# Performance work log

Measured on AMD Instinct MI355X. Metric: run time of the kernel, lower is better.

## Reference

```python
import jax, jax.numpy as jnp
import numpy as np

B, IN, OUT, L, R = 8192, 4096, 4096, 4, 128


def setup_inputs() -> dict:
    key = jax.random.key(0)
    ks = jax.random.split(key, 6)
    scale = 1.0 / np.sqrt(IN)
    return {
        "h_in": jax.random.normal(ks[0], (B, IN), dtype=jnp.float32),
        "S1s": jax.random.normal(ks[1], (L, IN, R), dtype=jnp.float32) * scale,
        "S2s": jax.random.normal(ks[2], (L, R, OUT), dtype=jnp.float32) * scale,
        "U1s": jax.random.normal(ks[3], (L, R, OUT), dtype=jnp.float32) / np.sqrt(R),
        "U2s": jax.random.normal(ks[4], (L, IN, R), dtype=jnp.float32) / np.sqrt(R),
        "bias": jax.random.normal(ks[5], (OUT,), dtype=jnp.float32) * scale,
    }


def reference(h_in, S1s, S2s, U1s, U2s, bias):
    l = S1s.shape[0]
    # term 1: x @ S1_i @ U1_i ; sketch to rank r then expand to out
    t1 = jnp.einsum("bi,lir->lbr", h_in, S1s)          # (l, B, r)
    y1 = jnp.einsum("lbr,lro->bo", t1, U1s)             # (B, out)
    # term 2: x @ U2_i @ S2_i
    t2 = jnp.einsum("bi,lir->lbr", h_in, U2s)          # (l, B, r)
    y2 = jnp.einsum("lbr,lro->bo", t2, S2s)             # (B, out)
    out = (y1 + y2) / (2.0 * l) + bias
    return out
```

## Files before the change

### kernel.cpp

```cpp
#include <hip/hip_runtime.h>


using bf16x8 = __attribute__((ext_vector_type(8))) __bf16;
using f32x4  = __attribute__((ext_vector_type(4))) float;

__device__ __forceinline__ unsigned short f2bf(float f) {
    union { float f; unsigned u; } c; c.f = f;
    unsigned u = c.u;
    return (unsigned short)((u + 0x7FFFu + ((u >> 16) & 1u)) >> 16);
}

__device__ __forceinline__ void gload_lds16(const void* g, void* l) {
    __builtin_amdgcn_global_load_lds((const __attribute__((address_space(1))) void*)g,
                                     (__attribute__((address_space(3))) void*)l,
                                     16, 0, 0);
}

__global__ void cvt_f32_to_bf16(const float4* __restrict__ src, ushort4* __restrict__ dst, int n4) {
    int i = blockIdx.x * blockDim.x + threadIdx.x;
    int stride = gridDim.x * blockDim.x;
    for (; i < n4; i += stride) {
        float4 v = src[i];
        ushort4 o;
        o.x = f2bf(v.x); o.y = f2bf(v.y); o.z = f2bf(v.z); o.w = f2bf(v.w);
        dst[i] = o;
    }
}

__global__ void pack_transpose(const float* __restrict__ p0, const float* __restrict__ p1,
                               unsigned short* __restrict__ dst,
                               int srcStride, int dstStride, long perT, long dstTOff) {
    const int t = blockIdx.z;
    const float* src = (t < 4) ? (p0 + (long)t * perT) : (p1 + (long)(t - 4) * perT);
    unsigned short* d = dst + (long)t * dstTOff;
    const int r0 = blockIdx.x * 32, c0 = blockIdx.y * 32;
    __shared__ float tile[32][33];
    const int tx = threadIdx.x & 31, ty = threadIdx.x >> 5;
#pragma unroll
    for (int j = 0; j < 4; ++j) {
        int rr = ty + j * 8;
        tile[rr][tx] = src[(long)(r0 + rr) * srcStride + c0 + tx];
    }
    __syncthreads();
#pragma unroll
    for (int j = 0; j < 4; ++j) {
        int cc = ty + j * 8;
        d[(long)(c0 + cc) * dstStride + r0 + tx] = f2bf(tile[tx][cc]);
    }
}

template <bool OUT_BF16>
__global__ __launch_bounds__(256) void gemm_bt(const unsigned short* __restrict__ A,
                                               const unsigned short* __restrict__ Bt,
                                               void* __restrict__ Cout,
                                               const float* __restrict__ bias,
                                               int M, int N, int K, float scale) {
    __shared__ unsigned short lA[128 * 32];
    __shared__ unsigned short lB[128 * 32];
    const int tid = threadIdx.x;
    const int wave = tid >> 6, lane = tid & 63;
    const int m0 = blockIdx.y * 128, n0 = blockIdx.x * 128;
    const int wm = wave >> 1, wn = wave & 1;

    f32x4 acc[4][4] = {};

    const unsigned short* gA = A + (size_t)(m0 + wave * 32 + (lane >> 2)) * K + (lane & 3) * 8;
    const unsigned short* gB = Bt + (size_t)(n0 + wave * 32 + (lane >> 2)) * K + (lane & 3) * 8;
    unsigned short* lA0 = &lA[(wave * 32) * 32];
    unsigned short* lB0 = &lB[(wave * 32) * 32];

    const unsigned short* pa = &lA[(wm * 64 + (lane & 15)) * 32 + (lane >> 4) * 8];
    const unsigned short* pb = &lB[(wn * 64 + (lane & 15)) * 32 + (lane >> 4) * 8];

    for (int kt = 0; kt < K; kt += 32) {
        gload_lds16(gA, lA0);
        gload_lds16(gA + (size_t)16 * K, lA0 + 16 * 32);
        gload_lds16(gB, lB0);
        gload_lds16(gB + (size_t)16 * K, lB0 + 16 * 32);
        __syncthreads();
        bf16x8 av[4], bv[4];
#pragma unroll
        for (int i = 0; i < 4; ++i) {
            av[i] = *(const bf16x8*)(pa + i * 16 * 32);
            bv[i] = *(const bf16x8*)(pb + i * 16 * 32);
        }
#pragma unroll
        for (int i = 0; i < 4; ++i)
#pragma unroll
            for (int j = 0; j < 4; ++j)
                acc[i][j] = __builtin_amdgcn_mfma_f32_16x16x32_bf16(av[i], bv[j], acc[i][j], 0, 0, 0);
        __syncthreads();
        gA += 32; gB += 32;
    }

    const int row0 = m0 + wm * 64, col0 = n0 + wn * 64;
    const int lr = (lane >> 4) * 4, lc = lane & 15;
    if (OUT_BF16) {
        unsigned short* Cb = (unsigned short*)Cout;
#pragma unroll
        for (int i = 0; i < 4; ++i)
#pragma unroll
            for (int j = 0; j < 4; ++j) {
                int col = col0 + j * 16 + lc;
#pragma unroll
                for (int q = 0; q < 4; ++q) {
                    int row = row0 + i * 16 + lr + q;
                    Cb[(size_t)row * N + col] = f2bf(acc[i][j][q]);
                }
            }
    } else {
        float* Cf = (float*)Cout;
#pragma unroll
        for (int i = 0; i < 4; ++i)
#pragma unroll
            for (int j = 0; j < 4; ++j) {
                int col = col0 + j * 16 + lc;
                float bv = bias[col];
#pragma unroll
                for (int q = 0; q < 4; ++q) {
                    int row = row0 + i * 16 + lr + q;
                    Cf[(size_t)row * N + col] = acc[i][j][q] * scale + bv;
                }
            }
    }
}

extern "C" void kernel_launch(void* const* d_in, const int* in_sizes, int n_in,
                              void* d_out, int out_size, void* d_ws, size_t ws_size,
                              hipStream_t stream) {
    const float* h_in = (const float*)d_in[0];
    const float* S1s  = (const float*)d_in[1];
    const float* S2s  = (const float*)d_in[2];
    const float* U1s  = (const float*)d_in[3];
    const float* U2s  = (const float*)d_in[4];
    const float* bias = (const float*)d_in[5];
    float* out = (float*)d_out;

    constexpr int B = 8192, IN = 4096, OUTD = 4096, R = 128;
    constexpr int NC = 1024;

    char* ws = (char*)d_ws;
    unsigned short* hB    = (unsigned short*)ws;
    unsigned short* AcatT = (unsigned short*)(ws + ((size_t)64 << 20));
    unsigned short* BcatT = (unsigned short*)(ws + ((size_t)72 << 20));
    unsigned short* T     = (unsigned short*)(ws + ((size_t)80 << 20));

    cvt_f32_to_bf16<<<2048, 256, 0, stream>>>((const float4*)h_in, (ushort4*)hB, B * IN / 4);

    pack_transpose<<<dim3(IN / 32, R / 32, 8), 256, 0, stream>>>(
        S1s, U2s, AcatT, R, IN, (long)IN * R, (long)R * IN);
    pack_transpose<<<dim3(R / 32, OUTD / 32, 8), 256, 0, stream>>>(
        U1s, S2s, BcatT, OUTD, NC, (long)R * OUTD, (long)R);

    gemm_bt<true><<<dim3(NC / 128, B / 128), 256, 0, stream>>>(hB, AcatT, (void*)T, nullptr,
                                                               B, NC, IN, 1.0f);
    gemm_bt<false><<<dim3(OUTD / 128, B / 128), 256, 0, stream>>>(T, BcatT, (void*)out, bias,
                                                                  B, OUTD, NC, 0.125f);
}
```

Baseline: 448.2 us.

## Replace GEMMs with 256x256 pipelined MFMA kernels, fuse input conversion, add split-K

Replaces the simple 128x128 single-buffered GEMM with a 512-thread 256x256-tile kernel. The new kernel double-buffers LDS with swizzled layouts, issues MFMA bursts at raised priority under explicit waitcnt and barrier scheduling, and swizzles workgroup order. The first GEMM reads the fp32 input directly and converts it to bf16 while staging into LDS, which removes the separate conversion pass. It uses split-K over two halves with a reduce+convert kernel afterwards. The second GEMM makes two N passes per workgroup and writes its output with nontemporal stores. This trades much more complex, shape-hardcoded code, heavy register pressure and an extra fp32 partial buffer for higher MFMA utilization and less global traffic.

```diff
diff --git a/kernel.cpp b/kernel.cpp
--- a/kernel.cpp
+++ b/kernel.cpp
@@ -2,6 +2,7 @@
 
 
 using bf16x8 = __attribute__((ext_vector_type(8))) __bf16;
+using u16x8  = __attribute__((ext_vector_type(8))) unsigned short;
 using f32x4  = __attribute__((ext_vector_type(4))) float;
 
 __device__ __forceinline__ unsigned short f2bf(float f) {
@@ -14,17 +15,6 @@
     __builtin_amdgcn_global_load_lds((const __attribute__((address_space(1))) void*)g,
                                      (__attribute__((address_space(3))) void*)l,
                                      16, 0, 0);
-}
-
-__global__ void cvt_f32_to_bf16(const float4* __restrict__ src, ushort4* __restrict__ dst, int n4) {
-    int i = blockIdx.x * blockDim.x + threadIdx.x;
-    int stride = gridDim.x * blockDim.x;
-    for (; i < n4; i += stride) {
-        float4 v = src[i];
-        ushort4 o;
-        o.x = f2bf(v.x); o.y = f2bf(v.y); o.z = f2bf(v.z); o.w = f2bf(v.w);
-        dst[i] = o;
-    }
 }
 
 __global__ void pack_transpose(const float* __restrict__ p0, const float* __restrict__ p1,
@@ -49,80 +39,253 @@
     }
 }
 
-template <bool OUT_BF16>
-__global__ __launch_bounds__(256) void gemm_bt(const unsigned short* __restrict__ A,
-                                               const unsigned short* __restrict__ Bt,
-                                               void* __restrict__ Cout,
-                                               const float* __restrict__ bias,
-                                               int M, int N, int K, float scale) {
-    __shared__ unsigned short lA[128 * 32];
-    __shared__ unsigned short lB[128 * 32];
+__global__ void reduce_cvt(const float4* __restrict__ a, const float4* __restrict__ b,
+                           ushort4* __restrict__ o, int n4) {
+    int i = blockIdx.x * blockDim.x + threadIdx.x;
+    int stride = gridDim.x * blockDim.x;
+    for (; i < n4; i += stride) {
+        float4 x = a[i], y = b[i];
+        ushort4 r;
+        r.x = f2bf(x.x + y.x); r.y = f2bf(x.y + y.y);
+        r.z = f2bf(x.z + y.z); r.w = f2bf(x.w + y.w);
+        o[i] = r;
+    }
+}
+
+#define SB()   __builtin_amdgcn_s_barrier()
+#define SCB()  __builtin_amdgcn_sched_barrier(0)
+#define WVM0() { asm volatile("s_waitcnt vmcnt(0)" ::: "memory"); SCB(); }
+#define WVM4() { asm volatile("s_waitcnt vmcnt(4)" ::: "memory"); SCB(); }
+#define WVM8() { asm volatile("s_waitcnt vmcnt(8)" ::: "memory"); SCB(); }
+#define WLG()  { asm volatile("s_waitcnt lgkmcnt(0)" ::: "memory"); SCB(); }
+
+template <int NPASS, int OMODE>
+__global__ __launch_bounds__(512, 2) void gemm8p(const void* __restrict__ Aq,
+                                                 const unsigned short* __restrict__ Bt,
+                                                 float* __restrict__ Cf,
+                                                 const float* __restrict__ bias,
+                                                 const int ld, const int N, const float scale) {
+    constexpr bool FUSED = (OMODE == 0);
+    constexpr int BM = 256, BN = 256;
+    constexpr int KT = (NPASS == 2) ? 16 : 32;
+    constexpr int NTT = 32;
+    constexpr int KTSH = (NPASS == 2) ? 4 : 5;
+    constexpr int NSTEP = 2048;
+    constexpr int M = 8192;
+    constexpr int BUFB = 65536;
+    __shared__ __align__(128) char smem[2 * BUFB];
+
     const int tid = threadIdx.x;
-    const int wave = tid >> 6, lane = tid & 63;
-    const int m0 = blockIdx.y * 128, n0 = blockIdx.x * 128;
-    const int wm = wave >> 1, wn = wave & 1;
-
-    f32x4 acc[4][4] = {};
-
-    const unsigned short* gA = A + (size_t)(m0 + wave * 32 + (lane >> 2)) * K + (lane & 3) * 8;
-    const unsigned short* gB = Bt + (size_t)(n0 + wave * 32 + (lane >> 2)) * K + (lane & 3) * 8;
-    unsigned short* lA0 = &lA[(wave * 32) * 32];
-    unsigned short* lB0 = &lB[(wave * 32) * 32];
-
-    const unsigned short* pa = &lA[(wm * 64 + (lane & 15)) * 32 + (lane >> 4) * 8];
-    const unsigned short* pb = &lB[(wn * 64 + (lane & 15)) * 32 + (lane >> 4) * 8];
-
-    for (int kt = 0; kt < K; kt += 32) {
-        gload_lds16(gA, lA0);
-        gload_lds16(gA + (size_t)16 * K, lA0 + 16 * 32);
-        gload_lds16(gB, lB0);
-        gload_lds16(gB + (size_t)16 * K, lB0 + 16 * 32);
-        __syncthreads();
-        bf16x8 av[4], bv[4];
-#pragma unroll
-        for (int i = 0; i < 4; ++i) {
-            av[i] = *(const bf16x8*)(pa + i * 16 * 32);
-            bv[i] = *(const bf16x8*)(pb + i * 16 * 32);
+    const int w = tid >> 6, lane = tid & 63;
+    const int wm = w >> 2, wn = w & 3;
+
+    const int nwg = gridDim.x;
+    const int wg = blockIdx.x;
+    const int swz = (wg & 7) * (nwg >> 3) + (wg >> 3);
+    int m0, n0, kbase;
+    if constexpr (NPASS == 1) {
+        kbase = (swz & 1) * KT * 64;
+        n0 = ((swz >> 1) & 3) * BN;
+        m0 = (swz >> 3) * BM;
+        Cf += (size_t)(swz & 1) * M * (size_t)N;
+    } else {
+        kbase = 0;
+        n0 = (swz & 7) * BN;
+        m0 = (swz >> 3) * BM;
+    }
+
+    const int rl = lane >> 3;
+    const int csw = (lane & 7) ^ rl;
+    const unsigned short* gB = Bt + (size_t)(n0 + w * 8 + rl) * ld + kbase + csw * 8;
+    const unsigned short* gA16 = FUSED ? nullptr
+        : (const unsigned short*)Aq + (size_t)(m0 + w * 8 + rl) * ld + kbase + csw * 8;
+
+    const int R  = w * 16 + (lane >> 2);
+    const int cp = lane & 3;
+    const float* gAf = FUSED
+        ? (const float*)Aq + (size_t)(m0 + R) * ld + kbase + cp * 8 : nullptr;
+    const int sA0 = (R >> 3) * 1024 + (R & 7) * 128 + (((cp)     ^ (R & 7)) << 4);
+    const int sA1 = (R >> 3) * 1024 + (R & 7) * 128 + (((cp + 4) ^ (R & 7)) << 4);
+
+    const int aRB = wm * 16384 + (lane & 15) * 128;
+    const int bRB = 32768 + (wn >> 1) * 16384 + ((wn & 1) * 64 + (lane & 15)) * 128;
+    const int ch0 = (((lane >> 4) + 0) ^ (lane & 7)) << 4;
+    const int ch1 = (((lane >> 4) + 4) ^ (lane & 7)) << 4;
+
+    f32x4 acc[8][4] = {};
+
+#define STAGE_B(tt, h) {                                                                        \
+        const unsigned short* g_ = gB + ((size_t)((tt) >> KTSH) * NSTEP + (size_t)(h) * 128) * ld \
+                                      + ((tt) & (KT - 1)) * 64;                                 \
+        char* l_ = smem + ((tt) & 1) * BUFB + 32768 + (h) * 16384 + w * 1024;                   \
+        gload_lds16(g_, l_); gload_lds16(g_ + (size_t)64 * ld, l_ + 8192); }
+
+#define STAGE_A16(tt, h) {                                                                      \
+        const unsigned short* g_ = gA16 + (size_t)(h) * 128 * ld + ((tt) & (KT - 1)) * 64;      \
+        char* l_ = smem + ((tt) & 1) * BUFB + (h) * 16384 + w * 1024;                           \
+        gload_lds16(g_, l_); gload_lds16(g_ + (size_t)64 * ld, l_ + 8192); }
+
+#define ALOAD(tt, h) {                                                                          \
+        const float* g_ = gAf + (size_t)(h) * 128 * ld + ((tt) & (KT - 1)) * 64;                \
+        ar[h][0] = *(const float4*)(g_);      ar[h][1] = *(const float4*)(g_ + 4);              \
+        ar[h][2] = *(const float4*)(g_ + 32); ar[h][3] = *(const float4*)(g_ + 36); }
+
+#define AWRITE(tt, h) {                                                                         \
+        char* l_ = smem + ((tt) & 1) * BUFB + (h) * 16384;                                      \
+        u16x8 p0_, p1_;                                                                         \
+        p0_[0] = f2bf(ar[h][0].x); p0_[1] = f2bf(ar[h][0].y);                                   \
+        p0_[2] = f2bf(ar[h][0].z); p0_[3] = f2bf(ar[h][0].w);                                   \
+        p0_[4] = f2bf(ar[h][1].x); p0_[5] = f2bf(ar[h][1].y);                                   \
+        p0_[6] = f2bf(ar[h][1].z); p0_[7] = f2bf(ar[h][1].w);                                   \
+        p1_[0] = f2bf(ar[h][2].x); p1_[1] = f2bf(ar[h][2].y);                                   \
+        p1_[2] = f2bf(ar[h][2].z); p1_[3] = f2bf(ar[h][2].w);                                   \
+        p1_[4] = f2bf(ar[h][3].x); p1_[5] = f2bf(ar[h][3].y);                                   \
+        p1_[6] = f2bf(ar[h][3].z); p1_[7] = f2bf(ar[h][3].w);                                   \
+        *(u16x8*)(l_ + sA0) = p0_; *(u16x8*)(l_ + sA1) = p1_; }
+
+#define DUMP(p) {                                                                               \
+        const int lc_ = lane & 15, lr_ = (lane >> 4) * 4;                                       \
+        _Pragma("unroll") for (int fm_ = 0; fm_ < 8; ++fm_) {                                   \
+            const int row_ = m0 + wm * 128 + fm_ * 16 + lr_;                                    \
+            _Pragma("unroll") for (int q_ = 0; q_ < 4; ++q_) {                                  \
+                _Pragma("unroll") for (int fn_ = 0; fn_ < 4; ++fn_) {                           \
+                    const int col_ = n0 + (p) * NSTEP + wn * 64 + fn_ * 16 + lc_;               \
+                    if constexpr (OMODE == 0) {                                                 \
+                        Cf[(size_t)(row_ + q_) * N + col_] = acc[fm_][fn_][q_];                 \
+                    } else {                                                                    \
+                        __builtin_nontemporal_store(acc[fm_][fn_][q_] * scale + bias[col_],     \
+                                                    Cf + (size_t)(row_ + q_) * N + col_);       \
+                    } } } } }
+
+#define CLRACC() { _Pragma("unroll") for (int i_ = 0; i_ < 8; ++i_)                             \
+        _Pragma("unroll") for (int j_ = 0; j_ < 4; ++j_) acc[i_][j_] = (f32x4){0.f, 0.f, 0.f, 0.f}; }
+
+    if constexpr (FUSED) {
+        bf16x8 av4[4][2], bv[4][2];
+        float4 ar[2][4];
+
+#define LOADA4(c, mb) { _Pragma("unroll") for (int f_ = 0; f_ < 4; ++f_) {                      \
+            const char* p_ = smem + (c) * BUFB + aRB + ((mb) + f_) * 2048;                      \
+            av4[f_][0] = *(const bf16x8*)(p_ + ch0); av4[f_][1] = *(const bf16x8*)(p_ + ch1); } }
+#define LOADB2F(c, pb) { _Pragma("unroll") for (int f_ = 0; f_ < 2; ++f_) {                     \
+            const char* p_ = smem + (c) * BUFB + bRB + ((pb) * 2 + f_) * 2048;                  \
+            bv[(pb) * 2 + f_][0] = *(const bf16x8*)(p_ + ch0);                                  \
+            bv[(pb) * 2 + f_][1] = *(const bf16x8*)(p_ + ch1); } }
+#define BURST4(mb, nb) { __builtin_amdgcn_s_setprio(1);                                         \
+            _Pragma("unroll") for (int f_ = 0; f_ < 4; ++f_)                                    \
+            _Pragma("unroll") for (int g_ = 0; g_ < 2; ++g_) {                                  \
+                acc[(mb) + f_][(nb) + g_] = __builtin_amdgcn_mfma_f32_16x16x32_bf16(            \
+                    av4[f_][0], bv[(nb) + g_][0], acc[(mb) + f_][(nb) + g_], 0, 0, 0);          \
+                acc[(mb) + f_][(nb) + g_] = __builtin_amdgcn_mfma_f32_16x16x32_bf16(            \
+                    av4[f_][1], bv[(nb) + g_][1], acc[(mb) + f_][(nb) + g_], 0, 0, 0); }        \
+            __builtin_amdgcn_s_setprio(0); }
+
+        ALOAD(0, 0); ALOAD(0, 1);
+        AWRITE(0, 0); AWRITE(0, 1);
+        WLG();
+        STAGE_B(0, 0); STAGE_B(0, 1);
+        ALOAD(1, 0); ALOAD(1, 1);
+
+        for (int tt = 0; tt < NTT - 1; ++tt) {
+            const int c = tt & 1;
+            WVM8(); SB();
+            LOADA4(c, 0); LOADB2F(c, 0);
+            AWRITE(tt + 1, 0);
+            STAGE_B(tt + 1, 0);
+            SB(); WLG();
+            BURST4(0, 0);
+            SB();
+            LOADA4(c, 4); LOADB2F(c, 1);
+            AWRITE(tt + 1, 1);
+            STAGE_B(tt + 1, 1);
+            SB(); WLG();
+            BURST4(4, 2);
+            SB();
+            LOADA4(c, 0);
+            if (tt + 2 < NTT) ALOAD(tt + 2, 0);
+            SB(); WLG();
+            BURST4(0, 2);
+            SB();
+            LOADA4(c, 4);
+            if (tt + 2 < NTT) ALOAD(tt + 2, 1);
+            SB(); WLG();
+            BURST4(4, 0);
         }
-#pragma unroll
-        for (int i = 0; i < 4; ++i)
-#pragma unroll
-            for (int j = 0; j < 4; ++j)
-                acc[i][j] = __builtin_amdgcn_mfma_f32_16x16x32_bf16(av[i], bv[j], acc[i][j], 0, 0, 0);
-        __syncthreads();
-        gA += 32; gB += 32;
-    }
-
-    const int row0 = m0 + wm * 64, col0 = n0 + wn * 64;
-    const int lr = (lane >> 4) * 4, lc = lane & 15;
-    if (OUT_BF16) {
-        unsigned short* Cb = (unsigned short*)Cout;
-#pragma unroll
-        for (int i = 0; i < 4; ++i)
-#pragma unroll
-            for (int j = 0; j < 4; ++j) {
-                int col = col0 + j * 16 + lc;
-#pragma unroll
-                for (int q = 0; q < 4; ++q) {
-                    int row = row0 + i * 16 + lr + q;
-                    Cb[(size_t)row * N + col] = f2bf(acc[i][j][q]);
-                }
-            }
+        {
+            WVM0(); SB();
+            LOADA4(1, 0); LOADB2F(1, 0); SB(); WLG(); BURST4(0, 0); SB();
+            LOADA4(1, 4); LOADB2F(1, 1); SB(); WLG(); BURST4(4, 2); SB();
+            LOADA4(1, 0); SB(); WLG(); BURST4(0, 2); SB();
+            LOADA4(1, 4); SB(); WLG(); BURST4(4, 0);
+        }
+        DUMP(0);
+#undef LOADA4
+#undef LOADB2F
+#undef BURST4
     } else {
-        float* Cf = (float*)Cout;
-#pragma unroll
-        for (int i = 0; i < 4; ++i)
-#pragma unroll
-            for (int j = 0; j < 4; ++j) {
-                int col = col0 + j * 16 + lc;
-                float bv = bias[col];
-#pragma unroll
-                for (int q = 0; q < 4; ++q) {
-                    int row = row0 + i * 16 + lr + q;
-                    Cf[(size_t)row * N + col] = acc[i][j][q] * scale + bv;
-                }
-            }
-    }
+        bf16x8 av[8][2], bv[4][2];
+
+#define LOADA(c, base) { _Pragma("unroll") for (int f_ = 0; f_ < 4; ++f_) {                     \
+            const char* p_ = smem + (c) * BUFB + aRB + ((base) + f_) * 2048;                    \
+            av[(base) + f_][0] = *(const bf16x8*)(p_ + ch0);                                    \
+            av[(base) + f_][1] = *(const bf16x8*)(p_ + ch1); } }
+#define LOADB(c, base) { _Pragma("unroll") for (int f_ = 0; f_ < 2; ++f_) {                     \
+            const char* p_ = smem + (c) * BUFB + bRB + ((base) + f_) * 2048;                    \
+            bv[(base) + f_][0] = *(const bf16x8*)(p_ + ch0);                                    \
+            bv[(base) + f_][1] = *(const bf16x8*)(p_ + ch1); } }
+#define BURST(mb, nb) { __builtin_amdgcn_s_setprio(1);                                          \
+            _Pragma("unroll") for (int f_ = 0; f_ < 4; ++f_)                                    \
+            _Pragma("unroll") for (int g_ = 0; g_ < 2; ++g_) {                                  \
+                acc[(mb) + f_][(nb) + g_] = __builtin_amdgcn_mfma_f32_16x16x32_bf16(            \
+                    av[(mb) + f_][0], bv[(nb) + g_][0], acc[(mb) + f_][(nb) + g_], 0, 0, 0);    \
+                acc[(mb) + f_][(nb) + g_] = __builtin_amdgcn_mfma_f32_16x16x32_bf16(            \
+                    av[(mb) + f_][1], bv[(nb) + g_][1], acc[(mb) + f_][(nb) + g_], 0, 0, 0); }  \
+            __builtin_amdgcn_s_setprio(0); }
+
+        STAGE_A16(0, 0); STAGE_A16(0, 1);
+        STAGE_B(0, 0); STAGE_B(0, 1);
+        STAGE_A16(1, 0); STAGE_A16(1, 1);
+
+        for (int tt = 0; tt < NTT - 1; ++tt) {
+            const int c = tt & 1;
+            if (NPASS == 2 && tt == KT) { WVM0(); } else { WVM4(); }
+            SB();
+            LOADA(c, 0); LOADB(c, 0);
+            STAGE_B(tt + 1, 0);
+            SB(); WLG();
+            BURST(0, 0);
+            SB();
+            LOADA(c, 4); LOADB(c, 2);
+            STAGE_B(tt + 1, 1);
+            SB(); WLG();
+            BURST(4, 0);
+            SB();
+            if (tt + 2 < NTT) STAGE_A16(tt + 2, 0);
+            SB();
+            BURST(0, 2);
+            SB();
+            if (tt + 2 < NTT) STAGE_A16(tt + 2, 1);
+            SB();
+            BURST(4, 2);
+            if (NPASS == 2 && tt == KT - 1) { DUMP(0); CLRACC(); }
+        }
+        {
+            WVM0(); SB();
+            LOADA(1, 0); LOADB(1, 0); SB(); WLG(); BURST(0, 0); SB();
+            LOADA(1, 4); LOADB(1, 2); SB(); WLG(); BURST(4, 0); SB();
+            BURST(0, 2); SB(); BURST(4, 2);
+        }
+        DUMP(NPASS - 1);
+#undef LOADA
+#undef LOADB
+#undef BURST
+    }
+#undef STAGE_B
+#undef STAGE_A16
+#undef ALOAD
+#undef AWRITE
+#undef DUMP
+#undef CLRACC
 }
 
 extern "C" void kernel_launch(void* const* d_in, const int* in_sizes, int n_in,
@@ -140,20 +303,22 @@
     constexpr int NC = 1024;
 
     char* ws = (char*)d_ws;
-    unsigned short* hB    = (unsigned short*)ws;
-    unsigned short* AcatT = (unsigned short*)(ws + ((size_t)64 << 20));
-    unsigned short* BcatT = (unsigned short*)(ws + ((size_t)72 << 20));
-    unsigned short* T     = (unsigned short*)(ws + ((size_t)80 << 20));
-
-    cvt_f32_to_bf16<<<2048, 256, 0, stream>>>((const float4*)h_in, (ushort4*)hB, B * IN / 4);
+    unsigned short* AcatT = (unsigned short*)ws;
+    unsigned short* BcatT = (unsigned short*)(ws + ((size_t)8 << 20));
+    unsigned short* T     = (unsigned short*)(ws + ((size_t)16 << 20));
+    float*          Tp    = (float*)(ws + ((size_t)32 << 20));
 
     pack_transpose<<<dim3(IN / 32, R / 32, 8), 256, 0, stream>>>(
         S1s, U2s, AcatT, R, IN, (long)IN * R, (long)R * IN);
     pack_transpose<<<dim3(R / 32, OUTD / 32, 8), 256, 0, stream>>>(
         U1s, S2s, BcatT, OUTD, NC, (long)R * OUTD, (long)R);
 
-    gemm_bt<true><<<dim3(NC / 128, B / 128), 256, 0, stream>>>(hB, AcatT, (void*)T, nullptr,
-                                                               B, NC, IN, 1.0f);
-    gemm_bt<false><<<dim3(OUTD / 128, B / 128), 256, 0, stream>>>(T, BcatT, (void*)out, bias,
-                                                                  B, OUTD, NC, 0.125f);
-}
+    gemm8p<1, 0><<<dim3(256), 512, 0, stream>>>(
+        (const void*)h_in, AcatT, Tp, nullptr, IN, NC, 1.0f);
+
+    reduce_cvt<<<2048, 256, 0, stream>>>(
+        (const float4*)Tp, (const float4*)(Tp + (size_t)B * NC), (ushort4*)T, B * NC / 4);
+
+    gemm8p<2, 1><<<dim3(256), 512, 0, stream>>>(
+        (const void*)T, BcatT, out, bias, NC, OUTD, 0.125f);
+}
```

Result: faster. 434.9 us (-3.0%).
